# Optimization experiments

Hardware: AMD Instinct MI355X
Metric: run time of the kernel (lower is better)

## Reference

```python
import jax, jax.numpy as jnp
import numpy as np

TAU_M = 2.0   # membrane time constant
TAU_S = 1.0   # synaptic time constant (tau_m = 2*tau_s -> closed-form spike times)
THETA = 1.0   # firing threshold
T_MAX = 20.0  # times beyond this count as 'no spike' (inf)
EPS = 1e-6


def lif_forward(input_spike_times, input_spike_synapse_ids, Wff, Wrec, max_output_spikes):
    """Event-driven recurrent LIF solver.

    PSP kernel: w * (exp(-(t-ts)/TAU_M) - exp(-(t-ts)/TAU_S)).
    Membrane: V(t) = A*z - B*z^2 with z = exp(-t/TAU_M), where A, B accumulate
    w*exp(ts/TAU_M) and w*exp(ts/TAU_S) per processed event. Spike when V = THETA
    (quadratic in z). Reset-by-subtraction of THETA via the membrane kernel.
    Emitted spikes are re-injected through the recurrent weights as new events.
    """
    Bsz, S = input_spike_times.shape
    N = Wff.shape[0]
    M = int(max_output_spikes)
    # process input events in causal (time) order
    order = jnp.argsort(input_spike_times, axis=1)
    t_srt = jnp.take_along_axis(input_spike_times, order, axis=1)
    sid_srt = jnp.take_along_axis(input_spike_synapse_ids, order, axis=1)
    bidx = jnp.arange(Bsz)
    WffT = Wff.T   # (n_synapses, N): row s = weights from synapse s to all neurons
    WrecT = Wrec.T # (N, N): row j = weights from neuron j to all neurons

    def step(carry, _):
        A, Bacc, ptr, t_cur, out_t, out_id, cnt = carry
        ptr_c = jnp.clip(ptr, 0, S - 1)
        t_in = jnp.where(ptr < S, t_srt[bidx, ptr_c], jnp.inf)  # next input event
        sid = sid_srt[bidx, ptr_c]
        # next threshold crossing per neuron: solve A z - B z^2 = THETA
        disc = A * A - 4.0 * THETA * Bacc
        ok_d = (disc > 0.0) & (Bacc > 1e-12)
        sq = jnp.sqrt(jnp.where(ok_d, disc, 1.0))
        Bs = jnp.where(Bacc > 1e-12, Bacc, 1.0)
        z_cur = jnp.exp(-t_cur / TAU_M)[:, None]

        def root_time(z):
            ok = ok_d & (z > 1e-12) & (z < z_cur * (1.0 - EPS))  # strictly in the future
            zs = jnp.where(ok, z, 0.5)
            return jnp.where(ok, -TAU_M * jnp.log(zs), jnp.inf)

        t1 = root_time((A - sq) / (2.0 * Bs))
        t2 = root_time((A + sq) / (2.0 * Bs))
        t_cand = jnp.minimum(t1, t2)                      # (B, N)
        j = jnp.argmin(t_cand, axis=1)                    # earliest-spiking neuron
        t_spk = t_cand[bidx, j]
        emit = (t_spk < t_in) & (t_spk < T_MAX) & (cnt < M)
        consume = (~emit) & jnp.isfinite(t_in)
        any_ev = emit | consume
        t_ev = jnp.where(emit, t_spk, t_in)
        t_evs = jnp.where(any_ev, t_ev, 0.0)
        em = jnp.exp(t_evs / TAU_M)[:, None]
        es = jnp.exp(t_evs / TAU_S)[:, None]
        w_in = WffT[sid]   # (B, N)
        w_rec = WrecT[j]   # (B, N)
        reset = THETA * jax.nn.one_hot(j, N, dtype=A.dtype)
        dA = jnp.where(consume[:, None], w_in * em, 0.0) + jnp.where(emit[:, None], (w_rec - reset) * em, 0.0)
        dB = jnp.where(consume[:, None], w_in * es, 0.0) + jnp.where(emit[:, None], w_rec * es, 0.0)
        A = A + dA
        Bacc = Bacc + dB
        ptr = ptr + consume.astype(ptr.dtype)
        t_cur = jnp.where(any_ev, t_ev, t_cur)
        slot = jnp.clip(cnt, 0, M - 1)
        out_t = out_t.at[bidx, slot].set(jnp.where(emit, t_spk, out_t[bidx, slot]))
        out_id = out_id.at[bidx, slot].set(jnp.where(emit, j.astype(out_id.dtype), out_id[bidx, slot]))
        cnt = cnt + emit.astype(cnt.dtype)
        return (A, Bacc, ptr, t_cur, out_t, out_id, cnt), None

    init = (
        jnp.zeros((Bsz, N), jnp.float32),
        jnp.zeros((Bsz, N), jnp.float32),
        jnp.zeros((Bsz,), jnp.int32),
        jnp.zeros((Bsz,), jnp.float32),
        jnp.full((Bsz, M), jnp.inf, jnp.float32),
        jnp.full((Bsz, M), -1, jnp.int32),
        jnp.zeros((Bsz,), jnp.int32),
    )
    carry, _ = jax.lax.scan(step, init, None, length=S + M)
    return carry[4], carry[5]


def setup_inputs() -> dict:
    key = jax.random.key(0)
    k1, k2, k3, k4 = jax.random.split(key, 4)
    batch, max_in, n_neurons, n_synapses = 256, 256, 128, 256
    input_spike_times = jax.random.uniform(k1, (batch, max_in), dtype=jnp.float32)
    input_spike_synapse_ids = jax.random.randint(k2, (batch, max_in), 0, n_synapses, dtype=jnp.int32)
    # module init: randn + 1.0, rescaled so the membrane operates near threshold
    feedforward_weights = (jax.random.normal(k3, (n_neurons, n_synapses), jnp.float32) + 1.0) * (4.0 / n_synapses)
    recurrent_weights = (jax.random.normal(k4, (n_neurons, n_neurons), jnp.float32) + 1.0) * (1.0 / n_neurons)
    return {
        "input_spike_times": input_spike_times,
        "input_spike_synapse_ids": input_spike_synapse_ids,
        "feedforward_weights": feedforward_weights,
        "recurrent_weights": recurrent_weights,
        "max_output_spikes": 256,
    }


def reference(input_spike_times, input_spike_synapse_ids, feedforward_weights, recurrent_weights, max_output_spikes):
    return lif_forward(input_spike_times, input_spike_synapse_ids, feedforward_weights, recurrent_weights, max_output_spikes)
```

## Files before the change

kernel.cpp:

```cpp
#include <hip/hip_runtime.h>

namespace {

constexpr int BATCH = 256;
constexpr int S_IN  = 256;
constexpr int NNEUR = 128;
constexpr int NSYN  = 256;
constexpr int MOUT  = 256;
constexpr int WSTR  = 130;
constexpr float NO_SPIKE_T = 1.0e30f;
constexpr float K1  = 0.72134752044448170f;
constexpr float NL2 = -1.3862943611198906f;
constexpr float ZEPS = (float)(1.0 - 1e-6);
constexpr float Z20F = 4.5399929762484854e-05f;

constexpr int LDS_WREC  = NNEUR * WSTR * 4;
constexpr int LDS_EV    = LDS_WREC;
constexpr int LDS_SPK   = LDS_EV + 264 * 16;
constexpr int LDS_LT    = LDS_SPK + 256 * 8;
constexpr int LDS_TOTAL = LDS_LT + 1024;

__device__ __forceinline__ float hw_exp2(float x) { return __builtin_amdgcn_exp2f(x); }
__device__ __forceinline__ float hw_log2(float x) { return __builtin_amdgcn_logf(x); }
__device__ __forceinline__ float hw_rcp(float x)  { return __builtin_amdgcn_rcpf(x); }

__global__ void transpose_wff_kernel(const float* __restrict__ wff,
                                     float* __restrict__ wffT) {
    int i = blockIdx.x * blockDim.x + threadIdx.x;
    int s = i >> 7;
    int n = i & (NNEUR - 1);
    wffT[i] = wff[n * NSYN + s];
}

template <int CTRL>
__device__ __forceinline__ int dpp_imax(int v) {
    int t = __builtin_amdgcn_update_dpp(v, v, CTRL, 0xf, 0xf, false);
    return (t > v) ? t : v;
}

__device__ __forceinline__ int argmax_key(float zc, int idxl) {
    int key = (__builtin_bit_cast(int, zc) & ~127) | (127 - idxl);
    key = dpp_imax<0x111>(key);
    key = dpp_imax<0x112>(key);
    key = dpp_imax<0x114>(key);
    key = dpp_imax<0x118>(key);
    key = dpp_imax<0x142>(key);
    key = dpp_imax<0x143>(key);
    return key;
}

__device__ __forceinline__ float cand_z(float A, float B, float zlim) {
    float disc = __builtin_fmaf(A, A, -4.0f * B);
    float r2B  = hw_rcp(B + B);
    float sq   = __fsqrt_rn(disc);
    float z2 = (A + sq) * r2B;
    float z1 = (A - sq) * r2B;
    bool okd = (disc > 0.0f) & (B > 1e-12f);
    bool v2 = okd & (z2 > 1e-12f) & (z2 < zlim);
    bool v1 = okd & (z1 > 1e-12f) & (z1 < zlim);
    return v2 ? z2 : (v1 ? z1 : 0.0f);
}

__global__ __launch_bounds__(64, 1) void lif_event_kernel(
    const float* __restrict__ in_t,
    const int*   __restrict__ in_sid,
    const float* __restrict__ wff,
    const float* __restrict__ wffT,
    const float* __restrict__ wrec,
    int use_t,
    float* __restrict__ out_t,
    float* __restrict__ out_id)
{
    extern __shared__ char smem[];
    float*  wrecL = (float*)smem;
    float4* evL   = (float4*)(smem + LDS_EV);
    float2* spkL  = (float2*)(smem + LDS_SPK);
    float*  lt    = (float*)(smem + LDS_LT);

    const int b = blockIdx.x;
    const int lane = threadIdx.x;

    const float4* wrec4 = (const float4*)wrec;
    for (int i = lane; i < NNEUR * NNEUR / 4; i += 64) {
        float4 v = wrec4[i];
        int n  = i >> 5;
        int c0 = (i & 31) * 4;
        wrecL[(c0 + 0) * WSTR + n] = v.x;
        wrecL[(c0 + 1) * WSTR + n] = v.y;
        wrecL[(c0 + 2) * WSTR + n] = v.z;
        wrecL[(c0 + 3) * WSTR + n] = v.w;
    }

    float myt[4]; int mys[4];
    for (int q = 0; q < 4; ++q) {
        int k = lane + 64 * q;
        myt[q] = in_t[b * S_IN + k];
        mys[q] = in_sid[b * S_IN + k];
        lt[k] = myt[q];
    }
    __syncthreads();
    int rk[4] = {0, 0, 0, 0};
    for (int j = 0; j < S_IN; ++j) {
        float tj = lt[j];
        #pragma unroll
        for (int q = 0; q < 4; ++q)
            rk[q] += (tj < myt[q] || (tj == myt[q] && j < lane + 64 * q)) ? 1 : 0;
    }
    for (int q = 0; q < 4; ++q) {
        float t = myt[q];
        float zi = hw_exp2(-K1 * t);
        float e  = hw_exp2(K1 * t);
        evL[rk[q]] = make_float4(__builtin_bit_cast(float, mys[q]), zi, e, e * e);
    }
    if (lane < 8) evL[S_IN + lane] = make_float4(0.0f, 0.0f, 1.0f, 1.0f);
    __syncthreads();

    const int n0 = lane * 2;
    const int n1 = n0 + 1;

    float A0 = 0.f, A1 = 0.f, B0 = 0.f, B1 = 0.f;
    int ptr = 0, cnt = 0;
    float zlim = ZEPS;

    float4 evA = evL[0], evB = evL[1], evC = evL[2], evD = evL[3];
    float2 wA, wB, wC, wD;
    {
        int s0 = __builtin_bit_cast(int, evA.x);
        int s1 = __builtin_bit_cast(int, evB.x);
        int s2 = __builtin_bit_cast(int, evC.x);
        int s3 = __builtin_bit_cast(int, evD.x);
        if (use_t) {
            wA = *(const float2*)&wffT[s0 * NNEUR + n0];
            wB = *(const float2*)&wffT[s1 * NNEUR + n0];
            wC = *(const float2*)&wffT[s2 * NNEUR + n0];
            wD = *(const float2*)&wffT[s3 * NNEUR + n0];
        } else {
            wA = make_float2(wff[n0 * NSYN + s0], wff[n1 * NSYN + s0]);
            wB = make_float2(wff[n0 * NSYN + s1], wff[n1 * NSYN + s1]);
            wC = make_float2(wff[n0 * NSYN + s2], wff[n1 * NSYN + s2]);
            wD = make_float2(wff[n0 * NSYN + s3], wff[n1 * NSYN + s3]);
        }
    }

    while (ptr < S_IN && cnt < MOUT) {
        const float zb0 = cand_z(A0, B0, zlim);
        const float zb1 = cand_z(A1, B1, zlim);
        const float zc = fmaxf(zb0, zb1);
        const int idxl = (zb1 > zb0) ? n1 : n0;

        const float A0p = __builtin_fmaf(wA.x, evA.z, A0);
        const float A1p = __builtin_fmaf(wA.y, evA.z, A1);
        const float B0p = __builtin_fmaf(wA.x, evA.w, B0);
        const float B1p = __builtin_fmaf(wA.y, evA.w, B1);
        const float zlimA = ZEPS * evA.y;
        const float zb0p = cand_z(A0p, B0p, zlimA);
        const float zb1p = cand_z(A1p, B1p, zlimA);
        const float zcp = fmaxf(zb0p, zb1p);

        const int key = argmax_key(zc, idxl);

        const bool cross  = (zc  > evA.y) & (zc  > Z20F);
        const bool crossp = (zcp > evB.y) & (zcp > Z20F);
        const unsigned long long m  = __ballot(cross);
        const unsigned long long mp = __ballot(crossp);

        if (m != 0ull) {
            const int key63 = __builtin_amdgcn_readlane(key, 63);
            const int jn = 127 - (key63 & 127);
            const float zmax = __builtin_bit_cast(float, key63 & ~127);
            const float2 wr = *(const float2*)&wrecL[jn * WSTR + n0];
            const float em = hw_rcp(zmax);
            const float es = em * em;
            const float r0 = (n0 == jn) ? 1.0f : 0.0f;
            const float r1 = (n1 == jn) ? 1.0f : 0.0f;
            A0 = __builtin_fmaf(wr.x - r0, em, A0);
            A1 = __builtin_fmaf(wr.y - r1, em, A1);
            B0 = __builtin_fmaf(wr.x, es, B0);
            B1 = __builtin_fmaf(wr.y, es, B1);
            zlim = ZEPS * zmax;
            if (lane == 0)
                spkL[cnt] = make_float2(NL2 * hw_log2(zmax), (float)jn);
            ++cnt;
        } else {
            A0 = A0p; A1 = A1p; B0 = B0p; B1 = B1p;
            if (mp == 0ull && ptr + 1 < S_IN) {
                A0 = __builtin_fmaf(wB.x, evB.z, A0);
                A1 = __builtin_fmaf(wB.y, evB.z, A1);
                B0 = __builtin_fmaf(wB.x, evB.w, B0);
                B1 = __builtin_fmaf(wB.y, evB.w, B1);
                zlim = ZEPS * evB.y;
                ptr += 2;
                evA = evC; evB = evD; wA = wC; wB = wD;
                evC = evL[ptr + 2]; evD = evL[ptr + 3];
                const int s2 = __builtin_bit_cast(int, evC.x);
                const int s3 = __builtin_bit_cast(int, evD.x);
                if (use_t) {
                    wC = *(const float2*)&wffT[s2 * NNEUR + n0];
                    wD = *(const float2*)&wffT[s3 * NNEUR + n0];
                } else {
                    wC = make_float2(wff[n0 * NSYN + s2], wff[n1 * NSYN + s2]);
                    wD = make_float2(wff[n0 * NSYN + s3], wff[n1 * NSYN + s3]);
                }
            } else {
                zlim = zlimA;
                ptr += 1;
                evA = evB; evB = evC; evC = evD;
                wA = wB; wB = wC; wC = wD;
                evD = evL[ptr + 3];
                const int s3 = __builtin_bit_cast(int, evD.x);
                if (use_t) {
                    wD = *(const float2*)&wffT[s3 * NNEUR + n0];
                } else {
                    wD = make_float2(wff[n0 * NSYN + s3], wff[n1 * NSYN + s3]);
                }
            }
        }
    }

    for (int it2 = 0; it2 < MOUT && cnt < MOUT; ++it2) {
        const float zb0 = cand_z(A0, B0, zlim);
        const float zb1 = cand_z(A1, B1, zlim);
        const float zc = fmaxf(zb0, zb1);
        const int idxl = (zb1 > zb0) ? n1 : n0;
        const int key = argmax_key(zc, idxl);
        const unsigned long long m = __ballot(zc > Z20F);
        if (m == 0ull) break;
        const int key63 = __builtin_amdgcn_readlane(key, 63);
        const int jn = 127 - (key63 & 127);
        const float zmax = __builtin_bit_cast(float, key63 & ~127);
        const float2 wr = *(const float2*)&wrecL[jn * WSTR + n0];
        const float em = hw_rcp(zmax);
        const float es = em * em;
        const float r0 = (n0 == jn) ? 1.0f : 0.0f;
        const float r1 = (n1 == jn) ? 1.0f : 0.0f;
        A0 = __builtin_fmaf(wr.x - r0, em, A0);
        A1 = __builtin_fmaf(wr.y - r1, em, A1);
        B0 = __builtin_fmaf(wr.x, es, B0);
        B1 = __builtin_fmaf(wr.y, es, B1);
        zlim = ZEPS * zmax;
        if (lane == 0)
            spkL[cnt] = make_float2(NL2 * hw_log2(zmax), (float)jn);
        ++cnt;
    }

    __syncthreads();
    for (int k = lane; k < MOUT; k += 64) {
        float2 s = spkL[k];
        bool live = (k < cnt);
        out_t[b * MOUT + k]  = live ? s.x : NO_SPIKE_T;
        out_id[b * MOUT + k] = live ? s.y : -1.0f;
    }
}

}

extern "C" void kernel_launch(void* const* d_in, const int* in_sizes, int n_in,
                              void* d_out, int out_size, void* d_ws, size_t ws_size,
                              hipStream_t stream) {
    (void)in_sizes; (void)n_in; (void)out_size;
    const float* in_t   = (const float*)d_in[0];
    const int*   in_sid = (const int*)d_in[1];
    const float* wff    = (const float*)d_in[2];
    const float* wrec   = (const float*)d_in[3];

    float* out_t  = (float*)d_out;
    float* out_id = (float*)d_out + BATCH * MOUT;

    float* wffT = (float*)d_ws;
    const size_t need = (size_t)(NSYN * NNEUR) * sizeof(float);
    const int use_t = (ws_size >= need) ? 1 : 0;

    if (use_t) {
        transpose_wff_kernel<<<(NSYN * NNEUR) / 256, 256, 0, stream>>>(wff, wffT);
    }
    lif_event_kernel<<<BATCH, 64, LDS_TOTAL, stream>>>(in_t, in_sid, wff, wffT, wrec,
                                                       use_t, out_t, out_id);
}
```

Measured before the change: 179.7 us.

## Speculatively test up to four input events per step in LIF event loop

Widens the event-driven loop's lookahead from two to four input events. Each iteration computes candidate crossings after 0–3 pending events and advances ptr by up to 4 when no spike intervenes, cutting serial iterations on long input runs. The spike-only tail loop is unrolled twice and uses the readlane of the argmax key in place of a ballot for its termination test. This adds per-iteration ALU work and register pressure, and the extra speculation is wasted whenever a spike occurs early.

```diff
diff --git a/kernel.cpp b/kernel.cpp
--- a/kernel.cpp
+++ b/kernel.cpp
@@ -117,28 +117,106 @@
 
     const int n0 = lane * 2;
     const int n1 = n0 + 1;
+    const int KZ20 = __builtin_bit_cast(int, Z20F) & ~127;
 
     float A0 = 0.f, A1 = 0.f, B0 = 0.f, B1 = 0.f;
     int ptr = 0, cnt = 0;
     float zlim = ZEPS;
 
+#define LOADW(dst, sid_)                                                     \
+    do {                                                                     \
+        const int s_ = (sid_);                                               \
+        if (use_t) dst = *(const float2*)&wffT[s_ * NNEUR + n0];             \
+        else       dst = make_float2(wff[n0 * NSYN + s_], wff[n1 * NSYN + s_]); \
+    } while (0)
+
     float4 evA = evL[0], evB = evL[1], evC = evL[2], evD = evL[3];
     float2 wA, wB, wC, wD;
-    {
-        int s0 = __builtin_bit_cast(int, evA.x);
-        int s1 = __builtin_bit_cast(int, evB.x);
-        int s2 = __builtin_bit_cast(int, evC.x);
-        int s3 = __builtin_bit_cast(int, evD.x);
-        if (use_t) {
-            wA = *(const float2*)&wffT[s0 * NNEUR + n0];
-            wB = *(const float2*)&wffT[s1 * NNEUR + n0];
-            wC = *(const float2*)&wffT[s2 * NNEUR + n0];
-            wD = *(const float2*)&wffT[s3 * NNEUR + n0];
+    LOADW(wA, __builtin_bit_cast(int, evA.x));
+    LOADW(wB, __builtin_bit_cast(int, evB.x));
+    LOADW(wC, __builtin_bit_cast(int, evC.x));
+    LOADW(wD, __builtin_bit_cast(int, evD.x));
+
+    while (ptr + 4 <= S_IN && cnt < MOUT) {
+        const float zb0 = cand_z(A0, B0, zlim);
+        const float zb1 = cand_z(A1, B1, zlim);
+        const float zc = fmaxf(zb0, zb1);
+        const int idxl = (zb1 > zb0) ? n1 : n0;
+        const int key = argmax_key(zc, idxl);
+
+        const float A0p = __builtin_fmaf(wA.x, evA.z, A0);
+        const float A1p = __builtin_fmaf(wA.y, evA.z, A1);
+        const float B0p = __builtin_fmaf(wA.x, evA.w, B0);
+        const float B1p = __builtin_fmaf(wA.y, evA.w, B1);
+        const float zl1 = ZEPS * evA.y;
+        const float zc1 = fmaxf(cand_z(A0p, B0p, zl1), cand_z(A1p, B1p, zl1));
+
+        const float A0q = __builtin_fmaf(wB.x, evB.z, A0p);
+        const float A1q = __builtin_fmaf(wB.y, evB.z, A1p);
+        const float B0q = __builtin_fmaf(wB.x, evB.w, B0p);
+        const float B1q = __builtin_fmaf(wB.y, evB.w, B1p);
+        const float zl2 = ZEPS * evB.y;
+        const float zc2 = fmaxf(cand_z(A0q, B0q, zl2), cand_z(A1q, B1q, zl2));
+
+        const float A0r = __builtin_fmaf(wC.x, evC.z, A0q);
+        const float A1r = __builtin_fmaf(wC.y, evC.z, A1q);
+        const float B0r = __builtin_fmaf(wC.x, evC.w, B0q);
+        const float B1r = __builtin_fmaf(wC.y, evC.w, B1q);
+        const float zl3 = ZEPS * evC.y;
+        const float zc3 = fmaxf(cand_z(A0r, B0r, zl3), cand_z(A1r, B1r, zl3));
+
+        const unsigned long long m0 = __ballot((zc  > evA.y) & (zc  > Z20F));
+        const unsigned long long m1 = __ballot((zc1 > evB.y) & (zc1 > Z20F));
+        const unsigned long long m2 = __ballot((zc2 > evC.y) & (zc2 > Z20F));
+        const unsigned long long m3 = __ballot((zc3 > evD.y) & (zc3 > Z20F));
+
+        if (m0 != 0ull) {
+            const int key63 = __builtin_amdgcn_readlane(key, 63);
+            const int jn = 127 - (key63 & 127);
+            const float zmax = __builtin_bit_cast(float, key63 & ~127);
+            const float2 wr = *(const float2*)&wrecL[jn * WSTR + n0];
+            const float em = hw_rcp(zmax);
+            const float es = em * em;
+            const float r0 = (n0 == jn) ? 1.0f : 0.0f;
+            const float r1 = (n1 == jn) ? 1.0f : 0.0f;
+            A0 = __builtin_fmaf(wr.x - r0, em, A0);
+            A1 = __builtin_fmaf(wr.y - r1, em, A1);
+            B0 = __builtin_fmaf(wr.x, es, B0);
+            B1 = __builtin_fmaf(wr.y, es, B1);
+            zlim = ZEPS * zmax;
+            if (lane == 0)
+                spkL[cnt] = make_float2(NL2 * hw_log2(zmax), (float)jn);
+            ++cnt;
+        } else if (m1 != 0ull) {
+            A0 = A0p; A1 = A1p; B0 = B0p; B1 = B1p; zlim = zl1; ptr += 1;
+            evA = evB; evB = evC; evC = evD; wA = wB; wB = wC; wC = wD;
+            evD = evL[ptr + 3];
+            LOADW(wD, __builtin_bit_cast(int, evD.x));
+        } else if (m2 != 0ull) {
+            A0 = A0q; A1 = A1q; B0 = B0q; B1 = B1q; zlim = zl2; ptr += 2;
+            evA = evC; evB = evD; wA = wC; wB = wD;
+            evC = evL[ptr + 2]; evD = evL[ptr + 3];
+            LOADW(wC, __builtin_bit_cast(int, evC.x));
+            LOADW(wD, __builtin_bit_cast(int, evD.x));
+        } else if (m3 != 0ull) {
+            A0 = A0r; A1 = A1r; B0 = B0r; B1 = B1r; zlim = zl3; ptr += 3;
+            evA = evD; wA = wD;
+            evB = evL[ptr + 1]; evC = evL[ptr + 2]; evD = evL[ptr + 3];
+            LOADW(wB, __builtin_bit_cast(int, evB.x));
+            LOADW(wC, __builtin_bit_cast(int, evC.x));
+            LOADW(wD, __builtin_bit_cast(int, evD.x));
         } else {
-            wA = make_float2(wff[n0 * NSYN + s0], wff[n1 * NSYN + s0]);
-            wB = make_float2(wff[n0 * NSYN + s1], wff[n1 * NSYN + s1]);
-            wC = make_float2(wff[n0 * NSYN + s2], wff[n1 * NSYN + s2]);
-            wD = make_float2(wff[n0 * NSYN + s3], wff[n1 * NSYN + s3]);
+            A0 = __builtin_fmaf(wD.x, evD.z, A0r);
+            A1 = __builtin_fmaf(wD.y, evD.z, A1r);
+            B0 = __builtin_fmaf(wD.x, evD.w, B0r);
+            B1 = __builtin_fmaf(wD.y, evD.w, B1r);
+            zlim = ZEPS * evD.y; ptr += 4;
+            evA = evL[ptr + 0]; evB = evL[ptr + 1];
+            evC = evL[ptr + 2]; evD = evL[ptr + 3];
+            LOADW(wA, __builtin_bit_cast(int, evA.x));
+            LOADW(wB, __builtin_bit_cast(int, evB.x));
+            LOADW(wC, __builtin_bit_cast(int, evC.x));
+            LOADW(wD, __builtin_bit_cast(int, evD.x));
         }
     }
 
@@ -147,23 +225,8 @@
         const float zb1 = cand_z(A1, B1, zlim);
         const float zc = fmaxf(zb0, zb1);
         const int idxl = (zb1 > zb0) ? n1 : n0;
-
-        const float A0p = __builtin_fmaf(wA.x, evA.z, A0);
-        const float A1p = __builtin_fmaf(wA.y, evA.z, A1);
-        const float B0p = __builtin_fmaf(wA.x, evA.w, B0);
-        const float B1p = __builtin_fmaf(wA.y, evA.w, B1);
-        const float zlimA = ZEPS * evA.y;
-        const float zb0p = cand_z(A0p, B0p, zlimA);
-        const float zb1p = cand_z(A1p, B1p, zlimA);
-        const float zcp = fmaxf(zb0p, zb1p);
-
         const int key = argmax_key(zc, idxl);
-
-        const bool cross  = (zc  > evA.y) & (zc  > Z20F);
-        const bool crossp = (zcp > evB.y) & (zcp > Z20F);
-        const unsigned long long m  = __ballot(cross);
-        const unsigned long long mp = __ballot(crossp);
-
+        const unsigned long long m = __ballot((zc > evA.y) & (zc > Z20F));
         if (m != 0ull) {
             const int key63 = __builtin_amdgcn_readlane(key, 63);
             const int jn = 127 - (key63 & 127);
@@ -182,66 +245,71 @@
                 spkL[cnt] = make_float2(NL2 * hw_log2(zmax), (float)jn);
             ++cnt;
         } else {
-            A0 = A0p; A1 = A1p; B0 = B0p; B1 = B1p;
-            if (mp == 0ull && ptr + 1 < S_IN) {
-                A0 = __builtin_fmaf(wB.x, evB.z, A0);
-                A1 = __builtin_fmaf(wB.y, evB.z, A1);
-                B0 = __builtin_fmaf(wB.x, evB.w, B0);
-                B1 = __builtin_fmaf(wB.y, evB.w, B1);
-                zlim = ZEPS * evB.y;
-                ptr += 2;
-                evA = evC; evB = evD; wA = wC; wB = wD;
-                evC = evL[ptr + 2]; evD = evL[ptr + 3];
-                const int s2 = __builtin_bit_cast(int, evC.x);
-                const int s3 = __builtin_bit_cast(int, evD.x);
-                if (use_t) {
-                    wC = *(const float2*)&wffT[s2 * NNEUR + n0];
-                    wD = *(const float2*)&wffT[s3 * NNEUR + n0];
-                } else {
-                    wC = make_float2(wff[n0 * NSYN + s2], wff[n1 * NSYN + s2]);
-                    wD = make_float2(wff[n0 * NSYN + s3], wff[n1 * NSYN + s3]);
-                }
-            } else {
-                zlim = zlimA;
-                ptr += 1;
-                evA = evB; evB = evC; evC = evD;
-                wA = wB; wB = wC; wC = wD;
-                evD = evL[ptr + 3];
-                const int s3 = __builtin_bit_cast(int, evD.x);
-                if (use_t) {
-                    wD = *(const float2*)&wffT[s3 * NNEUR + n0];
-                } else {
-                    wD = make_float2(wff[n0 * NSYN + s3], wff[n1 * NSYN + s3]);
-                }
-            }
+            A0 = __builtin_fmaf(wA.x, evA.z, A0);
+            A1 = __builtin_fmaf(wA.y, evA.z, A1);
+            B0 = __builtin_fmaf(wA.x, evA.w, B0);
+            B1 = __builtin_fmaf(wA.y, evA.w, B1);
+            zlim = ZEPS * evA.y;
+            ++ptr;
+            evA = evB; evB = evC; evC = evD; wA = wB; wB = wC; wC = wD;
+            evD = evL[ptr + 3];
+            LOADW(wD, __builtin_bit_cast(int, evD.x));
         }
     }
 
-    for (int it2 = 0; it2 < MOUT && cnt < MOUT; ++it2) {
-        const float zb0 = cand_z(A0, B0, zlim);
-        const float zb1 = cand_z(A1, B1, zlim);
-        const float zc = fmaxf(zb0, zb1);
-        const int idxl = (zb1 > zb0) ? n1 : n0;
-        const int key = argmax_key(zc, idxl);
-        const unsigned long long m = __ballot(zc > Z20F);
-        if (m == 0ull) break;
-        const int key63 = __builtin_amdgcn_readlane(key, 63);
-        const int jn = 127 - (key63 & 127);
-        const float zmax = __builtin_bit_cast(float, key63 & ~127);
-        const float2 wr = *(const float2*)&wrecL[jn * WSTR + n0];
-        const float em = hw_rcp(zmax);
-        const float es = em * em;
-        const float r0 = (n0 == jn) ? 1.0f : 0.0f;
-        const float r1 = (n1 == jn) ? 1.0f : 0.0f;
-        A0 = __builtin_fmaf(wr.x - r0, em, A0);
-        A1 = __builtin_fmaf(wr.y - r1, em, A1);
-        B0 = __builtin_fmaf(wr.x, es, B0);
-        B1 = __builtin_fmaf(wr.y, es, B1);
-        zlim = ZEPS * zmax;
-        if (lane == 0)
-            spkL[cnt] = make_float2(NL2 * hw_log2(zmax), (float)jn);
-        ++cnt;
-    }
+    while (cnt < MOUT) {
+        {
+            const float zb0 = cand_z(A0, B0, zlim);
+            const float zb1 = cand_z(A1, B1, zlim);
+            const float zc = fmaxf(zb0, zb1);
+            const int idxl = (zb1 > zb0) ? n1 : n0;
+            const int key = argmax_key(zc, idxl);
+            const int key63 = __builtin_amdgcn_readlane(key, 63);
+            if ((key63 & ~127) <= KZ20) { cnt = -cnt; break; }
+            const int jn = 127 - (key63 & 127);
+            const float zmax = __builtin_bit_cast(float, key63 & ~127);
+            const float2 wr = *(const float2*)&wrecL[jn * WSTR + n0];
+            const float em = hw_rcp(zmax);
+            const float es = em * em;
+            const float r0 = (n0 == jn) ? 1.0f : 0.0f;
+            const float r1 = (n1 == jn) ? 1.0f : 0.0f;
+            A0 = __builtin_fmaf(wr.x - r0, em, A0);
+            A1 = __builtin_fmaf(wr.y - r1, em, A1);
+            B0 = __builtin_fmaf(wr.x, es, B0);
+            B1 = __builtin_fmaf(wr.y, es, B1);
+            zlim = ZEPS * zmax;
+            if (lane == 0)
+                spkL[cnt] = make_float2(NL2 * hw_log2(zmax), (float)jn);
+            ++cnt;
+        }
+        if (cnt >= MOUT) break;
+        {
+            const float zb0 = cand_z(A0, B0, zlim);
+            const float zb1 = cand_z(A1, B1, zlim);
+            const float zc = fmaxf(zb0, zb1);
+            const int idxl = (zb1 > zb0) ? n1 : n0;
+            const int key = argmax_key(zc, idxl);
+            const int key63 = __builtin_amdgcn_readlane(key, 63);
+            if ((key63 & ~127) <= KZ20) { cnt = -cnt; break; }
+            const int jn = 127 - (key63 & 127);
+            const float zmax = __builtin_bit_cast(float, key63 & ~127);
+            const float2 wr = *(const float2*)&wrecL[jn * WSTR + n0];
+            const float em = hw_rcp(zmax);
+            const float es = em * em;
+            const float r0 = (n0 == jn) ? 1.0f : 0.0f;
+            const float r1 = (n1 == jn) ? 1.0f : 0.0f;
+            A0 = __builtin_fmaf(wr.x - r0, em, A0);
+            A1 = __builtin_fmaf(wr.y - r1, em, A1);
+            B0 = __builtin_fmaf(wr.x, es, B0);
+            B1 = __builtin_fmaf(wr.y, es, B1);
+            zlim = ZEPS * zmax;
+            if (lane == 0)
+                spkL[cnt] = make_float2(NL2 * hw_log2(zmax), (float)jn);
+            ++cnt;
+        }
+    }
+    if (cnt < 0) cnt = -cnt;
+#undef LOADW
 
     __syncthreads();
     for (int k = lane; k < MOUT; k += 64) {
```

After: 173.7 us. 3.4% less time.
